# Performance work log

Hardware: AMD Instinct MI355X
Metric: run time of the kernel (lower is better)

Reference implementation:

```python
import jax, jax.numpy as jnp
import numpy as np

BINS = 256

def _conv_x(t, k):
    # t: [N,1,H,W], k: [3] tap filter along width, 'same' padding
    return jax.lax.conv_general_dilated(t, k.reshape(1, 1, 1, 3), (1, 1), [(0, 0), (1, 1)])

def _conv_y(t, k):
    # t: [N,1,H,W], k: [3] tap filter along height, 'same' padding
    return jax.lax.conv_general_dilated(t, k.reshape(1, 1, 3, 1), (1, 1), [(1, 1), (0, 0)])

def calc_invCR(x):
    # Vectorized equivalent of the per-slice torch.histc loop:
    # 256-bin histogram over [-1,1] per (batch*channel) slice, Shannon entropy in bits / 8.
    n, _, h, w = x.shape
    res = h * w
    xf = x.reshape(n, res)
    valid = ((xf >= -1.0) & (xf <= 1.0)).astype(jnp.float32)
    # bin index; value exactly == max (1.0) falls into the last bin, matching torch.histc
    bins = jnp.clip(jnp.floor((xf + 1.0) * (BINS / 2.0)), 0, BINS - 1).astype(jnp.int32)
    counts = jnp.zeros((n, BINS), jnp.float32).at[jnp.arange(n)[:, None], bins].add(valid)
    p = counts / res
    ent = jnp.sum(jnp.where(p > 0, -p * jnp.log2(jnp.where(p > 0, p, 1.0)), 0.0))
    return ent / (8.0 * n)

def _forward(x, px, ux, cx, rx, py, uy, cy, ry):
    b, c, h, w = x.shape
    img = x.reshape(b * c, 1, h, w)
    cur = img
    xos, yos = [], []
    for lvl in range(5):
        xe, xo = cur[:, :, :, ::2], cur[:, :, :, 1::2]
        xo = xo - _conv_x(xe, px)
        xe = xe + _conv_x(xo, ux)
        xo = xo - _conv_x(xe, cx)
        xe = xe + _conv_x(xo, rx)
        ye, yo = xe[:, :, ::2, :], xe[:, :, 1::2, :]
        yo = yo - _conv_y(ye, py)
        if lvl < 2:
            ye = ye + _conv_y(yo, uy)
        # levels 3-5 in the source apply update_y to the (discarded) x?e tensor
        # (`x3e = x3e + self.update_y(x3o)`); that result is never used, so it is a
        # no-op for the output and is faithfully omitted here.
        yo = yo - _conv_y(ye, cy)
        ye = ye + _conv_y(yo, ry)
        xos.append(xo)
        yos.append(yo)
        cur = ye
    out = cur
    for xo, yo in zip(reversed(xos), reversed(yos)):
        out = jnp.concatenate((jnp.concatenate((out, yo), axis=2), xo), axis=3)
    deltas = jnp.fmod(out + 1.0, 2.0) - 1.0  # wrap residuals into [-1,1]
    loss1 = 255.0 * jnp.sqrt(jnp.mean(jnp.square(deltas)))
    loss0 = 255.0 * jnp.sqrt(jnp.mean(jnp.square(img)))
    invCR0 = calc_invCR(img)
    invCR1 = calc_invCR(deltas)
    return loss1, loss0, invCR0, invCR1

def setup_inputs() -> dict:
    key = jax.random.key(0)
    ks = jax.random.split(key, 9)
    inp = {"x": jax.random.uniform(ks[0], (32, 3, 512, 512), jnp.float32)}
    for i, name in enumerate(["px", "ux", "cx", "rx", "py", "uy", "cy", "ry"]):
        inp[name] = 0.25 * jax.random.normal(ks[i + 1], (3,), jnp.float32)
    return inp

def reference(x, px, ux, cx, rx, py, uy, cy, ry):
    return _forward(x, px, ux, cx, rx, py, uy, cy, ry)
```

## Files before the change

### kernel.cpp

```cpp
#include <hip/hip_runtime.h>
#include <math.h>

#define NIMG 96
#define NSLOT 1024
#define RES_INV (1.0f / 262144.0f)

__device__ __forceinline__ float wrap1(float v) {
  float t = v + 1.0f;
  return t - 2.0f * truncf(t * 0.5f) - 1.0f;
}
__device__ __forceinline__ int bin_fast(float v) {
  int b = (int)fmaf(v, 128.0f, 128.0f);
  return (b > 255) ? 255 : b;
}

template<int P, int SEGP, int USE_UY, int DO_IMG>
__global__ void __launch_bounds__(256) klift_fused(
    const float* __restrict__ src, float* __restrict__ ye_out,
    const float* __restrict__ kpx, const float* __restrict__ kux,
    const float* __restrict__ kcx, const float* __restrict__ krx,
    const float* __restrict__ kpy, const float* __restrict__ kuy,
    const float* __restrict__ kcy, const float* __restrict__ kry,
    double* __restrict__ partial,
    unsigned* __restrict__ hist_img, unsigned* __restrict__ hist_delta)
{
  constexpr int W2 = 64 * P;
  constexpr int H2 = W2;
  constexpr int H  = 2 * H2;
  constexpr int NP = SEGP + 8;
  constexpr int NR = 2 * NP;
  constexpr int NITER = NR / 4;
  __shared__ float tile[NR][W2];
  __shared__ unsigned shd[2][256];
  __shared__ unsigned shi[2][256];

  const int t = threadIdx.x, w = t >> 6, lane = t & 63;
  const int hsel = w >> 1;
  const int img = blockIdx.y;
  const int R0 = blockIdx.x * SEGP;
  const int base_in = 2 * R0 - 8;

  shd[0][t] = 0; shd[1][t] = 0;
  if (DO_IMG) { shi[0][t] = 0; shi[1][t] = 0; }

  const float px0 = kpx[0], px1 = kpx[1], px2 = kpx[2];
  const float ux0 = kux[0], ux1 = kux[1], ux2 = kux[2];
  const float cx0 = kcx[0], cx1 = kcx[1], cx2 = kcx[2];
  const float rx0 = krx[0], rx1 = krx[1], rx2 = krx[2];
  const float py0 = kpy[0], py1 = kpy[1], py2 = kpy[2];
  const float uy0 = kuy[0], uy1 = kuy[1], uy2 = kuy[2];
  const float cy0 = kcy[0], cy1 = kcy[1], cy2 = kcy[2];
  const float ry0 = kry[0], ry1 = kry[1], ry2 = kry[2];

  const float* ip = src + (size_t)img * H * (2 * W2);
  float sqi = 0.f, sqd = 0.f;

  auto stepm = [&](float (&d)[P], float (&s)[P], float k0, float k1, float k2) {
    float L = __shfl_up(s[P - 1], 1); if (lane == 0) L = 0.f;
    float R = __shfl_down(s[0], 1);   if (lane == 63) R = 0.f;
    float prev = L;
#pragma unroll
    for (int j = 0; j < P; j++) {
      float nxt = (j == P - 1) ? R : s[(j + 1) < P ? (j + 1) : 0];
      d[j] = fmaf(k0, prev, fmaf(k1, s[j], fmaf(k2, nxt, d[j])));
      prev = s[j];
    }
  };

  const int wcol = (P == 4) ? ((lane ^ ((lane >> 3) & 7)) * 4)
                 : (P == 2) ? (lane * 2) : lane;

  float4 pA[NITER], pB[NITER];
#pragma unroll
  for (int i = 0; i < NITER; ++i) {
    const int gin = base_in + w + 4 * i;
    const int g = (gin < 0) ? 0 : ((gin >= H) ? (H - 1) : gin);
    const float* rp = ip + (size_t)g * (2 * W2) + lane * (2 * P);
    if (P == 1) { float2 v = *(const float2*)rp; pA[i].x = v.x; pA[i].y = v.y; }
    else {
      pA[i] = *(const float4*)rp;
      if (P == 4) pB[i] = *(const float4*)(rp + 4);
    }
  }
  if (blockIdx.x == 0 || blockIdx.x == gridDim.x - 1) {
#pragma unroll
    for (int i = 0; i < NITER; ++i) {
      const int gin = base_in + w + 4 * i;
      if ((unsigned)gin >= (unsigned)H) {
        pA[i] = make_float4(0.f, 0.f, 0.f, 0.f);
        if (P == 4) pB[i] = make_float4(0.f, 0.f, 0.f, 0.f);
      }
    }
  }
  __syncthreads();

#pragma unroll
  for (int i = 0; i < NITER; ++i) {
    const int lr = w + 4 * i;
    const bool owned = (i >= 2) && (i < NITER - 2);
    float e[P], o[P];
    e[0] = pA[i].x; o[0] = pA[i].y;
    if (P >= 2) { e[P > 1 ? 1 : 0] = pA[i].z; o[P > 1 ? 1 : 0] = pA[i].w; }
    if (P == 4) {
      e[P > 2 ? 2 : 0] = pB[i].x; o[P > 2 ? 2 : 0] = pB[i].y;
      e[P > 3 ? 3 : 0] = pB[i].z; o[P > 3 ? 3 : 0] = pB[i].w;
    }
    if (DO_IMG && owned) {
#pragma unroll
      for (int j = 0; j < P; j++) {
        sqi += e[j] * e[j] + o[j] * o[j];
        atomicAdd(&shi[hsel][bin_fast(e[j])], 1u);
        atomicAdd(&shi[hsel][bin_fast(o[j])], 1u);
      }
    }
    stepm(o, e, -px0, -px1, -px2);
    stepm(e, o,  ux0,  ux1,  ux2);
    stepm(o, e, -cx0, -cx1, -cx2);
    stepm(e, o,  rx0,  rx1,  rx2);
    if (P == 4) {
      *(float4*)&tile[lr][wcol] =
          make_float4(e[0], e[P > 1 ? 1 : 0], e[P > 2 ? 2 : 0], e[P > 3 ? 3 : 0]);
    } else if (P == 2) {
      *(float2*)&tile[lr][wcol] = make_float2(e[0], e[P > 1 ? 1 : 0]);
    } else {
      tile[lr][wcol] = e[0];
    }
    if (owned) {
#pragma unroll
      for (int j = 0; j < P; j++) {
        float d = wrap1(o[j]);
        sqd += d * d;
        atomicAdd(&shd[hsel][bin_fast(d)], 1u);
      }
    }
  }
  __syncthreads();

  {
    constexpr int NSP = 256 / W2;
    constexpr int LEN = SEGP / NSP;
    constexpr int WIN = LEN + 8;
    const int col = t % W2;
    const int half = t / W2;
    const int q0 = half * LEN;
    int colr;
    if (P == 4) {
      const int ch = (col >> 2) ^ ((col >> 5) & 7);
      colr = (ch << 2) | (col & 3);
    } else colr = col;

    float ee[WIN], oo[WIN];
#pragma unroll
    for (int q = 0; q < WIN; ++q) {
      ee[q] = tile[2 * (q0 + q)][colr];
      oo[q] = tile[2 * (q0 + q) + 1][colr];
    }
#pragma unroll
    for (int q = 0; q < WIN; ++q) {
      float U = (q > 0) ? ee[q - 1] : 0.f;
      float D = (q < WIN - 1) ? ee[q + 1] : 0.f;
      oo[q] = fmaf(-py0, U, fmaf(-py1, ee[q], fmaf(-py2, D, oo[q])));
    }
    if (USE_UY) {
#pragma unroll
      for (int q = 0; q < WIN; ++q) {
        float U = (q > 0) ? oo[q - 1] : 0.f;
        float D = (q < WIN - 1) ? oo[q + 1] : 0.f;
        ee[q] = fmaf(uy0, U, fmaf(uy1, oo[q], fmaf(uy2, D, ee[q])));
      }
    }
#pragma unroll
    for (int q = 0; q < WIN; ++q) {
      float U = (q > 0) ? ee[q - 1] : 0.f;
      float D = (q < WIN - 1) ? ee[q + 1] : 0.f;
      oo[q] = fmaf(-cy0, U, fmaf(-cy1, ee[q], fmaf(-cy2, D, oo[q])));
    }
#pragma unroll
    for (int q = 0; q < WIN; ++q) {
      float U = (q > 0) ? oo[q - 1] : 0.f;
      float D = (q < WIN - 1) ? oo[q + 1] : 0.f;
      ee[q] = fmaf(ry0, U, fmaf(ry1, oo[q], fmaf(ry2, D, ee[q])));
    }
    float* outp = ye_out + (size_t)img * H2 * W2 + col;
#pragma unroll
    for (int q = 4; q < 4 + LEN; ++q) {
      const int g = R0 + q0 + q - 4;
      float d = wrap1(oo[q]);
      sqd += d * d;
      atomicAdd(&shd[hsel][bin_fast(d)], 1u);
      outp[(size_t)g * W2] = ee[q];
    }
  }

  for (int off = 32; off; off >>= 1) {
    sqd += __shfl_down(sqd, off);
    if (DO_IMG) sqi += __shfl_down(sqi, off);
  }
  if (lane == 0) {
    const int bid = blockIdx.x + blockIdx.y * gridDim.x;
    const int slot = (bid * 4 + w) & (NSLOT - 1);
    atomicAdd(&partial[NSLOT + slot], (double)sqd);
    if (DO_IMG) atomicAdd(&partial[slot], (double)sqi);
  }
  __syncthreads();
  unsigned hd = shd[0][t] + shd[1][t];
  if (hd) atomicAdd(&hist_delta[img * 256 + t], hd);
  if (DO_IMG) {
    unsigned hi = shi[0][t] + shi[1][t];
    if (hi) atomicAdd(&hist_img[img * 256 + t], hi);
  }
}

__global__ void __launch_bounds__(256) klift_tail64(
    const float* __restrict__ src,
    const float* __restrict__ kpx, const float* __restrict__ kux,
    const float* __restrict__ kcx, const float* __restrict__ krx,
    const float* __restrict__ kpy, const float* __restrict__ kcy,
    const float* __restrict__ kry,
    double* __restrict__ partial, unsigned* __restrict__ hist_delta)
{
  __shared__ float tile[64][65];
  __shared__ unsigned shd[256];
  const int t = threadIdx.x;
  const int img = blockIdx.x;
  shd[t] = 0;

  const float* sp = src + (size_t)img * 64 * 64;
  for (int idx = t; idx < 64 * 16; idx += 256) {
    const int r = idx >> 4, c4 = (idx & 15) << 2;
    float4 v = *(const float4*)(sp + r * 64 + c4);
    tile[r][c4] = v.x; tile[r][c4 + 1] = v.y;
    tile[r][c4 + 2] = v.z; tile[r][c4 + 3] = v.w;
  }
  const float px0 = kpx[0], px1 = kpx[1], px2 = kpx[2];
  const float ux0 = kux[0], ux1 = kux[1], ux2 = kux[2];
  const float cx0 = kcx[0], cx1 = kcx[1], cx2 = kcx[2];
  const float rx0 = krx[0], rx1 = krx[1], rx2 = krx[2];
  const float pc0 = kpy[0] + kcy[0], pc1 = kpy[1] + kcy[1], pc2 = kpy[2] + kcy[2];
  const float ry0 = kry[0], ry1 = kry[1], ry2 = kry[2];
  float sqd = 0.f;
  __syncthreads();

  for (int l = 0; l < 2; ++l) {
    const int s = 1 << l, n = 64 >> l, half = n >> 1;
    const int totx = n * half;

    for (int idx = t; idx < totx; idx += 256) {
      const int r = (idx / half) * s, c = idx % half;
      float L = (c > 0) ? tile[r][(2 * c - 2) * s] : 0.f;
      float M = tile[r][2 * c * s];
      float R = (c < half - 1) ? tile[r][(2 * c + 2) * s] : 0.f;
      tile[r][(2 * c + 1) * s] -= px0 * L + px1 * M + px2 * R;
    }
    __syncthreads();
    for (int idx = t; idx < totx; idx += 256) {
      const int r = (idx / half) * s, c = idx % half;
      float L = (c > 0) ? tile[r][(2 * c - 1) * s] : 0.f;
      float M = tile[r][(2 * c + 1) * s];
      float R = (c < half - 1) ? tile[r][(2 * c + 3) * s] : 0.f;
      tile[r][2 * c * s] += ux0 * L + ux1 * M + ux2 * R;
    }
    __syncthreads();
    for (int idx = t; idx < totx; idx += 256) {
      const int r = (idx / half) * s, c = idx % half;
      float L = (c > 0) ? tile[r][(2 * c - 2) * s] : 0.f;
      float M = tile[r][2 * c * s];
      float R = (c < half - 1) ? tile[r][(2 * c + 2) * s] : 0.f;
      tile[r][(2 * c + 1) * s] -= cx0 * L + cx1 * M + cx2 * R;
    }
    __syncthreads();
    for (int idx = t; idx < totx; idx += 256) {
      const int r = (idx / half) * s, c = idx % half;
      float L = (c > 0) ? tile[r][(2 * c - 1) * s] : 0.f;
      float M = tile[r][(2 * c + 1) * s];
      float R = (c < half - 1) ? tile[r][(2 * c + 3) * s] : 0.f;
      tile[r][2 * c * s] += rx0 * L + rx1 * M + rx2 * R;
    }
    __syncthreads();
    for (int idx = t; idx < totx; idx += 256) {
      const int r = (idx / half) * s, c = idx % half;
      float d = wrap1(tile[r][(2 * c + 1) * s]);
      sqd += d * d;
      atomicAdd(&shd[bin_fast(d)], 1u);
    }
    const int toty = half * half;
    for (int idx = t; idx < toty; idx += 256) {
      const int r = idx / half, j = idx % half, col = j * 2 * s;
      float U = (r > 0) ? tile[(2 * r - 2) * s][col] : 0.f;
      float M = tile[(2 * r) * s][col];
      float D = (r < half - 1) ? tile[(2 * r + 2) * s][col] : 0.f;
      tile[(2 * r + 1) * s][col] -= pc0 * U + pc1 * M + pc2 * D;
    }
    __syncthreads();
    for (int idx = t; idx < toty; idx += 256) {
      const int r = idx / half, j = idx % half, col = j * 2 * s;
      float U = (r > 0) ? tile[(2 * r - 1) * s][col] : 0.f;
      float M = tile[(2 * r + 1) * s][col];
      float D = (r < half - 1) ? tile[(2 * r + 3) * s][col] : 0.f;
      tile[(2 * r) * s][col] += ry0 * U + ry1 * M + ry2 * D;
    }
    __syncthreads();
    for (int idx = t; idx < toty; idx += 256) {
      const int r = idx / half, j = idx % half, col = j * 2 * s;
      float d = wrap1(tile[(2 * r + 1) * s][col]);
      sqd += d * d;
      atomicAdd(&shd[bin_fast(d)], 1u);
      if (l == 1) {
        float d2 = wrap1(tile[(2 * r) * s][col]);
        sqd += d2 * d2;
        atomicAdd(&shd[bin_fast(d2)], 1u);
      }
    }
    __syncthreads();
  }

  for (int off = 32; off; off >>= 1) sqd += __shfl_down(sqd, off);
  __shared__ float swv[4];
  if ((t & 63) == 0) swv[t >> 6] = sqd;
  __syncthreads();
  if (t == 0) {
    double tot = (double)swv[0] + swv[1] + swv[2] + swv[3];
    atomicAdd(&partial[NSLOT + (img & (NSLOT - 1))], tot);
  }
  unsigned hd = shd[t];
  if (hd) atomicAdd(&hist_delta[img * 256 + t], hd);
}

__global__ void __launch_bounds__(256) kfinal(
    const double* __restrict__ partial,
    const unsigned* __restrict__ hist_img,
    const unsigned* __restrict__ hist_delta,
    float* __restrict__ out)
{
  __shared__ double sI[256], sD[256], sPi[256], sPd[256];
  const int t = threadIdx.x;
  double entI = 0.0, entD = 0.0;
  for (int img = 0; img < NIMG; ++img) {
    unsigned ci = hist_img[img * 256 + t];
    if (ci) { float p = (float)ci * RES_INV; entI += (double)(-p * log2f(p)); }
    unsigned cd = hist_delta[img * 256 + t];
    if (cd) { float p = (float)cd * RES_INV; entD += (double)(-p * log2f(p)); }
  }
  double pi = 0.0, pd = 0.0;
  for (int s = t; s < NSLOT; s += 256) {
    pi += partial[s];
    pd += partial[NSLOT + s];
  }
  sI[t] = entI; sD[t] = entD; sPi[t] = pi; sPd[t] = pd;
  __syncthreads();
  for (int s = 128; s; s >>= 1) {
    if (t < s) {
      sI[t] += sI[t + s]; sD[t] += sD[t + s];
      sPi[t] += sPi[t + s]; sPd[t] += sPd[t + s];
    }
    __syncthreads();
  }
  if (t == 0) {
    const double tot = (double)NIMG * 262144.0;
    out[0] = (float)(255.0 * sqrt(sPd[0] / tot));
    out[1] = (float)(255.0 * sqrt(sPi[0] / tot));
    out[2] = (float)(sI[0] / (8.0 * NIMG));
    out[3] = (float)(sD[0] / (8.0 * NIMG));
  }
}

extern "C" void kernel_launch(void* const* d_in, const int* in_sizes, int n_in,
                              void* d_out, int out_size, void* d_ws, size_t ws_size,
                              hipStream_t stream)
{
  const float* x  = (const float*)d_in[0];
  const float* px = (const float*)d_in[1];
  const float* ux = (const float*)d_in[2];
  const float* cx = (const float*)d_in[3];
  const float* rx = (const float*)d_in[4];
  const float* py = (const float*)d_in[5];
  const float* uy = (const float*)d_in[6];
  const float* cy = (const float*)d_in[7];
  const float* ry = (const float*)d_in[8];
  float* out = (float*)d_out;

  char* ws = (char*)d_ws;
  double*   partial    = (double*)ws;
  unsigned* hist_img   = (unsigned*)(ws + 2 * NSLOT * 8);
  unsigned* hist_delta = (unsigned*)(ws + 2 * NSLOT * 8 + NIMG * 256 * 4);
  float* buf0 = (float*)(ws + (1 << 20));
  float* buf1 = (float*)(ws + (1 << 20) + ((size_t)32 << 20));
  float* buf2 = (float*)(ws + (1 << 20) + ((size_t)40 << 20));

  hipMemsetAsync(ws, 0, 2 * NSLOT * 8 + 2 * NIMG * 256 * 4, stream);

  klift_fused<4, 8, 1, 1><<<dim3(32, NIMG), 256, 0, stream>>>(
      x, buf0, px, ux, cx, rx, py, uy, cy, ry, partial, hist_img, hist_delta);
  klift_fused<2, 8, 1, 0><<<dim3(16, NIMG), 256, 0, stream>>>(
      buf0, buf1, px, ux, cx, rx, py, uy, cy, ry, partial, hist_img, hist_delta);
  klift_fused<1, 8, 0, 0><<<dim3(8, NIMG), 256, 0, stream>>>(
      buf1, buf2, px, ux, cx, rx, py, uy, cy, ry, partial, hist_img, hist_delta);
  klift_tail64<<<NIMG, 256, 0, stream>>>(buf2, px, ux, cx, rx, py, cy, ry,
                                         partial, hist_delta);
  kfinal<<<1, 256, 0, stream>>>(partial, hist_img, hist_delta, out);
}
```

Baseline: 89.58 us.

## Stage input rows into LDS via global_load_lds instead of register prefetch

Replaces the per-thread register prefetch of all input rows with direct global-to-LDS 16-byte async loads into a raw row buffer twice the old tile's width. Rows outside the image are zero-filled in LDS. The x-lifting results are then written back in place into that buffer with an unswizzled layout. This frees many registers (pA/pB arrays) and may raise occupancy, but doubles LDS use per block and drops the bank-conflict swizzle, which may cause conflicts in the vertical pass reads.

```diff
diff --git a/kernel.cpp b/kernel.cpp
--- a/kernel.cpp
+++ b/kernel.cpp
@@ -12,6 +12,13 @@
 __device__ __forceinline__ int bin_fast(float v) {
   int b = (int)fmaf(v, 128.0f, 128.0f);
   return (b > 255) ? 255 : b;
+}
+
+__device__ __forceinline__ void gload_lds16(const void* g, void* l) {
+  __builtin_amdgcn_global_load_lds(
+      (const __attribute__((address_space(1))) void*)g,
+      (__attribute__((address_space(3))) void*)l,
+      16, 0, 0);
 }
 
 template<int P, int SEGP, int USE_UY, int DO_IMG>
@@ -30,7 +37,10 @@
   constexpr int NP = SEGP + 8;
   constexpr int NR = 2 * NP;
   constexpr int NITER = NR / 4;
-  __shared__ float tile[NR][W2];
+  constexpr int ROWB = 2 * W2 * 4;
+  constexpr int NC = NR * ROWB / 1024;
+  constexpr int CPW = NC / 4;
+  __shared__ float raw[NR][2 * W2];
   __shared__ unsigned shd[2][256];
   __shared__ unsigned shi[2][256];
 
@@ -55,6 +65,27 @@
   const float* ip = src + (size_t)img * H * (2 * W2);
   float sqi = 0.f, sqd = 0.f;
 
+  {
+    const bool interior = (base_in >= 0) && (base_in + NR <= H);
+    const char* gb = (const char*)ip + (long)base_in * ROWB;
+    char* lb = (char*)&raw[0][0];
+#pragma unroll
+    for (int k = 0; k < CPW; ++k) {
+      const int q = w * CPW + k;
+      bool inb = interior;
+      if (!interior) {
+        const int r = base_in + ((P == 4) ? (q >> 1) : (P == 2) ? q : (2 * q));
+        inb = ((unsigned)r < (unsigned)H);
+      }
+      if (inb) {
+        gload_lds16(gb + (size_t)q * 1024 + (size_t)lane * 16, lb + q * 1024);
+      } else {
+        *(float4*)(lb + q * 1024 + lane * 16) = make_float4(0.f, 0.f, 0.f, 0.f);
+      }
+    }
+  }
+  __syncthreads();
+
   auto stepm = [&](float (&d)[P], float (&s)[P], float k0, float k1, float k2) {
     float L = __shfl_up(s[P - 1], 1); if (lane == 0) L = 0.f;
     float R = __shfl_down(s[0], 1);   if (lane == 63) R = 0.f;
@@ -67,43 +98,25 @@
     }
   };
 
-  const int wcol = (P == 4) ? ((lane ^ ((lane >> 3) & 7)) * 4)
-                 : (P == 2) ? (lane * 2) : lane;
-
-  float4 pA[NITER], pB[NITER];
-#pragma unroll
-  for (int i = 0; i < NITER; ++i) {
-    const int gin = base_in + w + 4 * i;
-    const int g = (gin < 0) ? 0 : ((gin >= H) ? (H - 1) : gin);
-    const float* rp = ip + (size_t)g * (2 * W2) + lane * (2 * P);
-    if (P == 1) { float2 v = *(const float2*)rp; pA[i].x = v.x; pA[i].y = v.y; }
-    else {
-      pA[i] = *(const float4*)rp;
-      if (P == 4) pB[i] = *(const float4*)(rp + 4);
-    }
-  }
-  if (blockIdx.x == 0 || blockIdx.x == gridDim.x - 1) {
-#pragma unroll
-    for (int i = 0; i < NITER; ++i) {
-      const int gin = base_in + w + 4 * i;
-      if ((unsigned)gin >= (unsigned)H) {
-        pA[i] = make_float4(0.f, 0.f, 0.f, 0.f);
-        if (P == 4) pB[i] = make_float4(0.f, 0.f, 0.f, 0.f);
-      }
-    }
-  }
-  __syncthreads();
-
 #pragma unroll
   for (int i = 0; i < NITER; ++i) {
     const int lr = w + 4 * i;
     const bool owned = (i >= 2) && (i < NITER - 2);
     float e[P], o[P];
-    e[0] = pA[i].x; o[0] = pA[i].y;
-    if (P >= 2) { e[P > 1 ? 1 : 0] = pA[i].z; o[P > 1 ? 1 : 0] = pA[i].w; }
     if (P == 4) {
-      e[P > 2 ? 2 : 0] = pB[i].x; o[P > 2 ? 2 : 0] = pB[i].y;
-      e[P > 3 ? 3 : 0] = pB[i].z; o[P > 3 ? 3 : 0] = pB[i].w;
+      float4 v0 = *(float4*)&raw[lr][lane * 8];
+      float4 v1 = *(float4*)&raw[lr][lane * 8 + 4];
+      e[0] = v0.x; o[0] = v0.y;
+      e[P > 1 ? 1 : 0] = v0.z; o[P > 1 ? 1 : 0] = v0.w;
+      e[P > 2 ? 2 : 0] = v1.x; o[P > 2 ? 2 : 0] = v1.y;
+      e[P > 3 ? 3 : 0] = v1.z; o[P > 3 ? 3 : 0] = v1.w;
+    } else if (P == 2) {
+      float4 v0 = *(float4*)&raw[lr][lane * 4];
+      e[0] = v0.x; o[0] = v0.y;
+      e[P > 1 ? 1 : 0] = v0.z; o[P > 1 ? 1 : 0] = v0.w;
+    } else {
+      float2 v = *(float2*)&raw[lr][lane * 2];
+      e[0] = v.x; o[0] = v.y;
     }
     if (DO_IMG && owned) {
 #pragma unroll
@@ -118,12 +131,12 @@
     stepm(o, e, -cx0, -cx1, -cx2);
     stepm(e, o,  rx0,  rx1,  rx2);
     if (P == 4) {
-      *(float4*)&tile[lr][wcol] =
+      *(float4*)&raw[lr][lane * 8] =
           make_float4(e[0], e[P > 1 ? 1 : 0], e[P > 2 ? 2 : 0], e[P > 3 ? 3 : 0]);
     } else if (P == 2) {
-      *(float2*)&tile[lr][wcol] = make_float2(e[0], e[P > 1 ? 1 : 0]);
+      *(float2*)&raw[lr][lane * 4] = make_float2(e[0], e[P > 1 ? 1 : 0]);
     } else {
-      tile[lr][wcol] = e[0];
+      raw[lr][lane * 2] = e[0];
     }
     if (owned) {
 #pragma unroll
@@ -143,17 +156,14 @@
     const int col = t % W2;
     const int half = t / W2;
     const int q0 = half * LEN;
-    int colr;
-    if (P == 4) {
-      const int ch = (col >> 2) ^ ((col >> 5) & 7);
-      colr = (ch << 2) | (col & 3);
-    } else colr = col;
+    const int cidx = (P == 4) ? ((col >> 2) * 8 + (col & 3))
+                   : (P == 2) ? ((col >> 1) * 4 + (col & 1)) : (col * 2);
 
     float ee[WIN], oo[WIN];
 #pragma unroll
     for (int q = 0; q < WIN; ++q) {
-      ee[q] = tile[2 * (q0 + q)][colr];
-      oo[q] = tile[2 * (q0 + q) + 1][colr];
+      ee[q] = raw[2 * (q0 + q)][cidx];
+      oo[q] = raw[2 * (q0 + q) + 1][cidx];
     }
 #pragma unroll
     for (int q = 0; q < WIN; ++q) {
```

Result: slower. 115.6 us (+29.1%).
